# Performance work log

Hardware: AMD Instinct MI355X
Metric: run time of the kernel (lower is better)

Reference implementation:

```python
import jax, jax.numpy as jnp
from jax import lax
import numpy as np

# --- config (torchvision Mask R-CNN RPN / RoIAlign defaults) ---
IMG = 800.0        # image size (square)
STRIDE = 4.0       # FPN level stride -> feature 200x200
K_PRE = 2000       # pre-NMS top-k proposals
K_POST = 512       # post-NMS proposals kept
IOU_THR = 0.7      # RPN NMS IoU threshold
OUT = 7            # RoIAlign output size
SR = 2             # RoIAlign sampling ratio
SCALE = 1.0 / STRIDE
BBOX_XFORM_CLIP = 4.135166556742356  # log(1000/16)


def setup_inputs() -> dict:
    key = jax.random.key(0)
    k1, k2, k3 = jax.random.split(key, 3)
    C, H, W = 256, 200, 200
    feature = jax.random.normal(k1, (C, H, W), jnp.float32)
    # anchor grid: 3 sizes per location, stride 4 (proper geometric anchors)
    sizes = np.array([32.0, 64.0, 128.0], np.float32)
    ys, xs = np.meshgrid(np.arange(H, dtype=np.float32) * STRIDE,
                         np.arange(W, dtype=np.float32) * STRIDE, indexing='ij')
    ctr = np.stack([xs, ys], axis=-1).reshape(-1, 1, 2)            # [HW,1,2] (x,y)
    half = np.stack([sizes / 2, sizes / 2], axis=-1)[None]          # [1,3,2]
    anchors = np.concatenate([ctr - half + 0 * half, ctr + half], axis=-1)
    anchors = np.broadcast_to(np.concatenate([ctr - half, ctr + half], -1),
                              (H * W, 3, 4)).reshape(-1, 4).astype(np.float32)
    N = anchors.shape[0]  # 120000
    objectness = jax.random.normal(k2, (N,), jnp.float32)
    deltas = jax.random.normal(k3, (N, 4), jnp.float32) * 0.1
    return {"feature": feature, "objectness": objectness,
            "deltas": deltas, "anchors": jnp.asarray(anchors)}


def decode_boxes(deltas, anchors):
    w = anchors[:, 2] - anchors[:, 0]
    h = anchors[:, 3] - anchors[:, 1]
    cx = anchors[:, 0] + 0.5 * w
    cy = anchors[:, 1] + 0.5 * h
    dx, dy = deltas[:, 0], deltas[:, 1]
    dw = jnp.minimum(deltas[:, 2], BBOX_XFORM_CLIP)
    dh = jnp.minimum(deltas[:, 3], BBOX_XFORM_CLIP)
    pcx = dx * w + cx
    pcy = dy * h + cy
    pw = jnp.exp(dw) * w
    ph = jnp.exp(dh) * h
    boxes = jnp.stack([pcx - 0.5 * pw, pcy - 0.5 * ph,
                       pcx + 0.5 * pw, pcy + 0.5 * ph], axis=-1)
    return jnp.clip(boxes, 0.0, IMG)


def pairwise_iou(b):  # b: [K,4]
    area = (b[:, 2] - b[:, 0]) * (b[:, 3] - b[:, 1])
    lt = jnp.maximum(b[:, None, :2], b[None, :, :2])
    rb = jnp.minimum(b[:, None, 2:], b[None, :, 2:])
    wh = jnp.maximum(rb - lt, 0.0)
    inter = wh[..., 0] * wh[..., 1]
    return inter / (area[:, None] + area[None, :] - inter + 1e-6)


def nms_suppress(boxes_sorted, iou_thr):
    # boxes sorted by descending score; returns keep mask [K]
    K = boxes_sorted.shape[0]
    iou = pairwise_iou(boxes_sorted)
    js = jnp.arange(K)
    def body(i, supp):
        row = (iou[i] > iou_thr) & (js > i)
        return jnp.where(supp[i], supp, supp | row)
    supp = lax.fori_loop(0, K, body, jnp.zeros((K,), bool))
    return ~supp


def roi_align(feature, boxes):
    # feature: [C,H,W]; boxes: [M,4] in image coords; aligned=False variant
    C, H, W = feature.shape
    P = OUT * SR
    def one(box):
        x1, y1, x2, y2 = box[0] * SCALE, box[1] * SCALE, box[2] * SCALE, box[3] * SCALE
        rw = jnp.maximum(x2 - x1, 1.0)
        rh = jnp.maximum(y2 - y1, 1.0)
        idx = jnp.arange(P, dtype=feature.dtype) + 0.5
        ys = y1 + idx * (rh / P)   # [P]
        xs = x1 + idx * (rw / P)
        yy, xx = jnp.meshgrid(ys, xs, indexing='ij')     # [P,P]
        y = jnp.clip(yy, 0.0, H - 1.0)
        x = jnp.clip(xx, 0.0, W - 1.0)
        y0 = jnp.floor(y).astype(jnp.int32)
        x0 = jnp.floor(x).astype(jnp.int32)
        y1i = jnp.minimum(y0 + 1, H - 1)
        x1i = jnp.minimum(x0 + 1, W - 1)
        ly = y - y0.astype(feature.dtype)
        lx = x - x0.astype(feature.dtype)
        v00 = feature[:, y0, x0]    # [C,P,P]
        v01 = feature[:, y0, x1i]
        v10 = feature[:, y1i, x0]
        v11 = feature[:, y1i, x1i]
        val = (v00 * (1 - ly) * (1 - lx) + v01 * (1 - ly) * lx
               + v10 * ly * (1 - lx) + v11 * ly * lx)  # [C,P,P]
        return val.reshape(C, OUT, SR, OUT, SR).mean(axis=(2, 4))  # [C,7,7]
    return jax.vmap(one)(boxes)


def reference(feature, objectness, deltas, anchors):
    boxes = decode_boxes(deltas, anchors)                    # [N,4]
    scores, idx = lax.top_k(objectness, K_PRE)               # pre-NMS top-k
    cand = boxes[idx]                                        # [K_PRE,4] sorted
    keep = nms_suppress(cand, IOU_THR)                       # [K_PRE] bool
    masked = jnp.where(keep, scores, -jnp.inf)
    _, fidx = lax.top_k(masked, K_POST)                      # post-NMS top-k
    final_boxes = cand[fidx]                                 # [K_POST,4]
    valid = keep[fidx].astype(feature.dtype)                 # [K_POST]
    roi = roi_align(feature, final_boxes)                    # [K_POST,256,7,7]
    return roi * valid[:, None, None, None]
```

## Files before the change

### kernel.cpp

```cpp
#include <hip/hip_runtime.h>
#include <cstdint>
#include <cstddef>

#define N_ANCH   120000
#define K_PRE    2000
#define K_POST   512
#define CAP      4096
#define NWORD    32
#define HBINS    4096
#define IOU_THR  0.7f
#define IMGF     800.0f
#define CLIPV    4.135166556742356f
#define FH       200
#define FW       200
#define FC       256
#define SCALE    0.25f

#define TROWS    96
#define NTILE    21
#define CH       8

#define CG       16
#define TPE      4


typedef unsigned long long u64;
typedef float f2u __attribute__((ext_vector_type(2), aligned(4)));

struct Ws {
    uint32_t T;
    uint32_t cnt;
    int32_t  nk;
    uint32_t pad;
    u64      combo[CAP];
    float4   cand[K_PRE];
    int      rows[K_POST];
    u64      mask[(size_t)K_PRE * NWORD];
};

__device__ inline uint32_t fkey(float f) {
    uint32_t u = __float_as_uint(f);
    return (u & 0x80000000u) ? ~u : (u | 0x80000000u);
}

__global__ __launch_bounds__(1024) void zero_k(Ws* __restrict__ ws) {
    uint32_t* h = (uint32_t*)ws->mask;
    for (int i = threadIdx.x; i < HBINS; i += 1024) h[i] = 0u;
    if (threadIdx.x == 0) { ws->cnt = 0u; ws->nk = 0; ws->T = 0u; }
}

__global__ __launch_bounds__(256) void th_k(const float* __restrict__ feat,
                                            const float* __restrict__ obj,
                                            float* __restrict__ featT,
                                            uint32_t* __restrict__ hist) {
    __shared__ float tile[32][257];
    __shared__ uint32_t h[HBINS];
    const int tid = threadIdx.x, bid = blockIdx.x;

    if (bid < 118) {
        for (int i = tid; i < HBINS; i += 256) h[i] = 0u;
        __syncthreads();
        const int i = bid * 256 + tid;
        if (i < N_ANCH / 4) {
            float4 v = ((const float4*)obj)[i];
            atomicAdd(&h[fkey(v.x) >> 20], 1u);
            atomicAdd(&h[fkey(v.y) >> 20], 1u);
            atomicAdd(&h[fkey(v.z) >> 20], 1u);
            atomicAdd(&h[fkey(v.w) >> 20], 1u);
        }
        __syncthreads();
        for (int i2 = tid; i2 < HBINS; i2 += 256)
            if (h[i2]) atomicAdd(&hist[i2], h[i2]);
    }

    const int P0 = bid * 32;
    const int pl = tid & 31, c0 = tid >> 5;
#pragma unroll
    for (int k = 0; k < 32; ++k)
        tile[pl][k * 8 + c0] = feat[(size_t)(k * 8 + c0) * (FH * FW) + P0 + pl];
    __syncthreads();
#pragma unroll
    for (int m = 0; m < 32; ++m)
        featT[(size_t)(P0 + m) * FC + tid] = tile[m][tid];
}

__global__ __launch_bounds__(256) void hist_k(const float* __restrict__ obj,
                                              uint32_t* __restrict__ hist) {
    __shared__ uint32_t h[HBINS];
    for (int i = threadIdx.x; i < HBINS; i += 256) h[i] = 0u;
    __syncthreads();
    const float4* o4 = (const float4*)obj;
    for (int i = blockIdx.x * 256 + threadIdx.x; i < N_ANCH / 4; i += gridDim.x * 256) {
        float4 v = o4[i];
        atomicAdd(&h[fkey(v.x) >> 20], 1u);
        atomicAdd(&h[fkey(v.y) >> 20], 1u);
        atomicAdd(&h[fkey(v.z) >> 20], 1u);
        atomicAdd(&h[fkey(v.w) >> 20], 1u);
    }
    __syncthreads();
    for (int i = threadIdx.x; i < HBINS; i += 256)
        if (h[i]) atomicAdd(&hist[i], h[i]);
}

__global__ __launch_bounds__(256) void gather_k(const float* __restrict__ obj,
                                                const uint32_t* __restrict__ hist,
                                                Ws* __restrict__ ws) {
    __shared__ uint32_t wsum[4];
    __shared__ uint32_t sT;
    const int tid = threadIdx.x;
    const int lane = tid & 63, wave = tid >> 6;
    uint32_t c[16]; uint32_t s = 0;
#pragma unroll
    for (int k = 0; k < 16; ++k) { c[k] = hist[HBINS - 1 - (16 * tid + k)]; s += c[k]; }
    uint32_t incl = s;
    for (int off = 1; off < 64; off <<= 1) {
        uint32_t t = __shfl_up(incl, off);
        if (lane >= off) incl += t;
    }
    if (lane == 63) wsum[wave] = incl;
    __syncthreads();
    uint32_t wpre = 0;
    for (int w2 = 0; w2 < wave; ++w2) wpre += wsum[w2];
    uint32_t before = wpre + incl - s;
#pragma unroll
    for (int k = 0; k < 16; ++k) {
        uint32_t after = before + c[k];
        if (before < K_PRE && after >= K_PRE)
            sT = (uint32_t)(HBINS - 1 - (16 * tid + k)) << 20;
        before = after;
    }
    __syncthreads();
    const uint32_t T = sT;
    int i = blockIdx.x * 256 + tid;
    if (i >= N_ANCH / 4) return;
    float4 v = ((const float4*)obj)[i];
    float vals[4] = {v.x, v.y, v.z, v.w};
#pragma unroll
    for (int k = 0; k < 4; ++k) {
        uint32_t u = fkey(vals[k]);
        if (u >= T) {
            uint32_t pos = atomicAdd(&ws->cnt, 1u);
            if (pos < CAP)
                ws->combo[pos] = ((u64)(~u) << 32) | (uint32_t)(4 * i + k);
        }
    }
}

__global__ __launch_bounds__(256) void rank_decode_k(const float* __restrict__ deltas,
                                                     const float* __restrict__ anchors,
                                                     Ws* __restrict__ ws) {
    __shared__ u64 sc[CAP];
    const int tid = threadIdx.x;
    int M = (int)ws->cnt;
    if (M > CAP) M = CAP;
    const int ebase = blockIdx.x * (256 / TPE);
    if (ebase >= M) return;
    for (int e = tid; e < M; e += 256) sc[e] = ws->combo[e];
    __syncthreads();
    const int gid = ebase + tid / TPE;
    const int sub = tid & (TPE - 1);
    if (gid >= M) return;
    const u64 mine = sc[gid];
    int cnt = 0;
    int j = sub;
    for (; j + 3 * TPE < M; j += 4 * TPE) {
        u64 a = sc[j], b = sc[j + TPE], c = sc[j + 2 * TPE], d = sc[j + 3 * TPE];
        cnt += (int)(a < mine) + (int)(b < mine) + (int)(c < mine) + (int)(d < mine);
    }
    for (; j < M; j += TPE) cnt += (int)(sc[j] < mine);
    cnt += __shfl_xor(cnt, 1);
    cnt += __shfl_xor(cnt, 2);
    if (sub == 0 && cnt < K_PRE) {
        const uint32_t idx = (uint32_t)(mine & 0xFFFFFFFFull);
        float a0 = anchors[idx * 4 + 0], a1 = anchors[idx * 4 + 1];
        float a2 = anchors[idx * 4 + 2], a3 = anchors[idx * 4 + 3];
        float d0 = deltas[idx * 4 + 0],  d1 = deltas[idx * 4 + 1];
        float d2 = fminf(deltas[idx * 4 + 2], CLIPV);
        float d3 = fminf(deltas[idx * 4 + 3], CLIPV);
        float w = a2 - a0, h = a3 - a1;
        float cx = a0 + 0.5f * w, cy = a1 + 0.5f * h;
        float pcx = d0 * w + cx, pcy = d1 * h + cy;
        float pw = expf(d2) * w, ph = expf(d3) * h;
        float x1 = fminf(fmaxf(pcx - 0.5f * pw, 0.0f), IMGF);
        float y1 = fminf(fmaxf(pcy - 0.5f * ph, 0.0f), IMGF);
        float x2 = fminf(fmaxf(pcx + 0.5f * pw, 0.0f), IMGF);
        float y2 = fminf(fmaxf(pcy + 0.5f * ph, 0.0f), IMGF);
        ws->cand[cnt] = make_float4(x1, y1, x2, y2);
    }
}

__global__ __launch_bounds__(256) void nms_mask_k(Ws* __restrict__ ws) {
    const int i = blockIdx.x;
    const int lane = threadIdx.x & 63;
    const int wave = threadIdx.x >> 6;
    const float4 bi = ws->cand[i];
    const float ai = (bi.z - bi.x) * (bi.w - bi.y);
    for (int wd = wave; wd < NWORD; wd += 4) {
        int j = wd * 64 + lane;
        bool bit = false;
        if (j < K_PRE && j > i) {
            float4 bj = ws->cand[j];
            float aj = (bj.z - bj.x) * (bj.w - bj.y);
            float xx1 = fmaxf(bi.x, bj.x);
            float yy1 = fmaxf(bi.y, bj.y);
            float xx2 = fminf(bi.z, bj.z);
            float yy2 = fminf(bi.w, bj.w);
            float ww = fmaxf(xx2 - xx1, 0.0f);
            float hh = fmaxf(yy2 - yy1, 0.0f);
            float inter = ww * hh;
            float iou = inter / (ai + aj - inter + 1e-6f);
            bit = iou > IOU_THR;
        }
        u64 bal = __ballot(bit);
        if (lane == 0) ws->mask[(size_t)i * NWORD + wd] = bal;
    }
}

__global__ __launch_bounds__(512) void nms_scan_k(Ws* __restrict__ ws) {
    __shared__ __align__(16) u64 sbuf[2][TROWS * NWORD];
    __shared__ int s_stop;
    const int tid = threadIdx.x;
    const int lane = tid & 63;
    const int wave = tid >> 6;
    const int lmod = lane & 31;
    const u64* __restrict__ mask = ws->mask;

    {
        const ulonglong2* src = (const ulonglong2*)mask;
        ulonglong2* dst = (ulonglong2*)sbuf[0];
        for (int e = tid; e < TROWS * NWORD / 2; e += 512) dst[e] = src[e];
    }
    if (tid == 0) s_stop = 0;
    __syncthreads();

    u64 supp = 0ull;
    int kcnt = 0;
    int decided = 0;
    for (int t = 0; t < NTILE; ++t) {
        const int base = t * TROWS;
        const int nb = min(TROWS, K_PRE - base);
        if (wave == 0) {
            const u64* sm = sbuf[t & 1];
            u64 A[CH], B[CH];
#pragma unroll
            for (int b = 0; b < CH; ++b) A[b] = sm[b * NWORD + lmod];
            for (int s = 0; s < nb; s += 2 * CH) {
                const bool hasB = (s + CH) < nb;
                if (hasB) {
#pragma unroll
                    for (int b = 0; b < CH; ++b) B[b] = sm[(s + CH + b) * NWORD + lmod];
                }
                {
                    const int w = (base + s) >> 6;
                    const int bofs = (base + s) & 63;
                    u64 keptw = 0ull;
                    if (lane == w) {
                        u64 cur = supp;
#pragma unroll
                        for (int b = 0; b < CH; ++b) {
                            u64 bit = (cur >> (bofs + b)) & 1ull;
                            u64 sel = bit - 1ull;
                            cur |= A[b] & sel;
                            keptw |= sel & (1ull << b);
                        }
                        supp = cur;
                    }
                    u64 kb = __shfl(keptw, w);
                    kcnt += __popcll(kb);
#pragma unroll
                    for (int b = 0; b < CH; ++b) {
                        u64 sel = 0ull - ((kb >> b) & 1ull);
                        supp |= A[b] & sel;
                    }
                }
                if (hasB) {
                    if (s + 2 * CH < nb) {
#pragma unroll
                        for (int b = 0; b < CH; ++b)
                            A[b] = sm[(s + 2 * CH + b) * NWORD + lmod];
                    }
                    const int w = (base + s + CH) >> 6;
                    const int bofs = (base + s + CH) & 63;
                    u64 keptw = 0ull;
                    if (lane == w) {
                        u64 cur = supp;
#pragma unroll
                        for (int b = 0; b < CH; ++b) {
                            u64 bit = (cur >> (bofs + b)) & 1ull;
                            u64 sel = bit - 1ull;
                            cur |= B[b] & sel;
                            keptw |= sel & (1ull << b);
                        }
                        supp = cur;
                    }
                    u64 kb = __shfl(keptw, w);
                    kcnt += __popcll(kb);
#pragma unroll
                    for (int b = 0; b < CH; ++b) {
                        u64 sel = 0ull - ((kb >> b) & 1ull);
                        supp |= B[b] & sel;
                    }
                }
            }
            decided = base + nb;
            if (lane == 0 && kcnt >= K_POST) s_stop = 1;
        } else if (t + 1 < NTILE) {
            const int nbase = (t + 1) * TROWS;
            const int npairs = (min(TROWS, K_PRE - nbase) * NWORD) / 2;
            const ulonglong2* src = (const ulonglong2*)(mask + (size_t)nbase * NWORD);
            ulonglong2* dst = (ulonglong2*)sbuf[(t + 1) & 1];
            for (int e = tid - 64; e < npairs; e += 448) dst[e] = src[e];
        }
        __syncthreads();
        if (s_stop) break;
    }

    if (wave == 0) {
        u64 valid;
        if (lane < NWORD - 1)       valid = ~0ull;
        else if (lane == NWORD - 1) valid = (1ull << (K_PRE - (NWORD - 1) * 64)) - 1ull;
        else                        valid = 0ull;
        const int dw = decided - lane * 64;
        const u64 dmask = (dw <= 0) ? 0ull : ((dw >= 64) ? ~0ull : ((1ull << dw) - 1ull));
        u64 keepw = (~supp) & valid & dmask;
        int cnt = __popcll(keepw);
        int incl = cnt;
        for (int off = 1; off < 64; off <<= 1) {
            int t = __shfl_up(incl, off);
            if (lane >= off) incl += t;
        }
        int pos = incl - cnt;
        u64 kw = keepw;
        while (kw) {
            int b = __ffsll((unsigned long long)kw) - 1;
            kw &= kw - 1ull;
            if (pos < K_POST) ws->rows[pos] = lane * 64 + b;
            ++pos;
        }
        int total = __shfl(incl, 63);
        if (lane == 0) ws->nk = total;
        int start = total < K_POST ? total : K_POST;
        for (int r = start + lane; r < K_POST; r += 64) ws->rows[r] = -1;
    }
}

__global__ __launch_bounds__(256) void roi2_k(const float* __restrict__ featT,
                                              const Ws* __restrict__ ws,
                                              float* __restrict__ out) {
    __shared__ float sout[CG * 49];
    const int b = blockIdx.x;
    const int xcd = b & 7;
    const int s = b >> 3;
    const int r = s & (K_POST - 1);
    const int cg = xcd + 8 * (s >> 9);
    const int cbase = cg * CG;
    float* oblk = out + (size_t)r * (FC * 49) + (size_t)cbase * 49;
    const int row = ws->rows[r];
    const int tid = threadIdx.x;

    if (row < 0) {
        for (int e = tid; e < CG * 49; e += 256) oblk[e] = 0.0f;
        return;
    }

    if (tid < 196) {
        const int p = tid >> 2;
        const int cq = tid & 3;
        const int oy = p / 7, ox = p % 7;

        const float4 bx = ws->cand[row];
        const float x1 = bx.x * SCALE, y1 = bx.y * SCALE;
        const float x2 = bx.z * SCALE, y2 = bx.w * SCALE;
        const float rw = fmaxf(x2 - x1, 1.0f);
        const float rh = fmaxf(y2 - y1, 1.0f);
        const float stepx = rw / 14.0f;
        const float stepy = rh / 14.0f;

        int    o0[4], o1[4];
        float4 w4[4];
#pragma unroll
        for (int sub = 0; sub < 4; ++sub) {
            const int sy = sub >> 1, sx = sub & 1;
            float yy = y1 + ((float)(2 * oy + sy) + 0.5f) * stepy;
            float y = fminf(fmaxf(yy, 0.0f), (float)(FH - 1));
            float fy0 = floorf(y);
            int iy0 = (int)fy0;
            int iy1 = min(iy0 + 1, FH - 1);
            float ly = y - fy0;
            float xx = x1 + ((float)(2 * ox + sx) + 0.5f) * stepx;
            float x = fminf(fmaxf(xx, 0.0f), (float)(FW - 1));
            float fx0 = floorf(x);
            int ix0 = (int)fx0;
            float lx = x - fx0;
            float wxl, wxr; int basex;
            if (ix0 >= FW - 1) { basex = FW - 2; wxl = 0.0f; wxr = 1.0f; }
            else               { basex = ix0;    wxl = 1.0f - lx; wxr = lx; }
            float wy0 = 1.0f - ly, wy1 = ly;
            o0[sub] = (iy0 * FW + basex) * FC;
            o1[sub] = (iy1 * FW + basex) * FC;
            w4[sub] = make_float4(wy0 * wxl * 0.25f, wy0 * wxr * 0.25f,
                                  wy1 * wxl * 0.25f, wy1 * wxr * 0.25f);
        }

        const int cofs = cbase + cq * 4;
        float4 v[16];
#pragma unroll
        for (int sub = 0; sub < 4; ++sub) {
            v[4 * sub + 0] = *(const float4*)(featT + (size_t)o0[sub] + cofs);
            v[4 * sub + 1] = *(const float4*)(featT + (size_t)o0[sub] + FC + cofs);
            v[4 * sub + 2] = *(const float4*)(featT + (size_t)o1[sub] + cofs);
            v[4 * sub + 3] = *(const float4*)(featT + (size_t)o1[sub] + FC + cofs);
        }

        float ax = 0.0f, ay = 0.0f, az = 0.0f, aw = 0.0f;
#pragma unroll
        for (int sub = 0; sub < 4; ++sub) {
            const float4 w = w4[sub];
            ax += w.x * v[4*sub].x + w.y * v[4*sub+1].x + w.z * v[4*sub+2].x + w.w * v[4*sub+3].x;
            ay += w.x * v[4*sub].y + w.y * v[4*sub+1].y + w.z * v[4*sub+2].y + w.w * v[4*sub+3].y;
            az += w.x * v[4*sub].z + w.y * v[4*sub+1].z + w.z * v[4*sub+2].z + w.w * v[4*sub+3].z;
            aw += w.x * v[4*sub].w + w.y * v[4*sub+1].w + w.z * v[4*sub+2].w + w.w * v[4*sub+3].w;
        }
        sout[(cq * 4 + 0) * 49 + p] = ax;
        sout[(cq * 4 + 1) * 49 + p] = ay;
        sout[(cq * 4 + 2) * 49 + p] = az;
        sout[(cq * 4 + 3) * 49 + p] = aw;
    }
    __syncthreads();
    for (int e = tid; e < CG * 49; e += 256) oblk[e] = sout[e];
}

__global__ __launch_bounds__(256) void roi_k(const float* __restrict__ feat,
                                             const Ws* __restrict__ ws,
                                             float* __restrict__ out) {
    const int b = blockIdx.x;
    const int xcd = b & 7;
    const int s = b >> 3;
    const int r = s & (K_POST - 1);
    const int cg = xcd + 8 * (s >> 9);
    const int cbase = cg * CG;
    float* oblk = out + (size_t)r * (FC * 49) + (size_t)cbase * 49;
    const int row = ws->rows[r];
    const int tid = threadIdx.x;

    if (row < 0) {
        for (int e = tid; e < CG * 49; e += 256) oblk[e] = 0.0f;
        return;
    }
    if (tid >= 245) return;

    const int p = tid % 49;
    const int cslot = tid / 49;
    const int oy = p / 7, ox = p % 7;

    const float4 bx = ws->cand[row];
    const float x1 = bx.x * SCALE, y1 = bx.y * SCALE;
    const float x2 = bx.z * SCALE, y2 = bx.w * SCALE;
    const float rw = fmaxf(x2 - x1, 1.0f);
    const float rh = fmaxf(y2 - y1, 1.0f);
    const float stepx = rw / 14.0f;
    const float stepy = rh / 14.0f;

    int    off0[4], off1[4];
    float4 w4[4];
#pragma unroll
    for (int sub = 0; sub < 4; ++sub) {
        const int sy = sub >> 1, sx = sub & 1;
        float yy = y1 + ((float)(2 * oy + sy) + 0.5f) * stepy;
        float y = fminf(fmaxf(yy, 0.0f), (float)(FH - 1));
        float fy0 = floorf(y);
        int iy0 = (int)fy0;
        int iy1 = min(iy0 + 1, FH - 1);
        float ly = y - fy0;
        float xx = x1 + ((float)(2 * ox + sx) + 0.5f) * stepx;
        float x = fminf(fmaxf(xx, 0.0f), (float)(FW - 1));
        float fx0 = floorf(x);
        int ix0 = (int)fx0;
        float lx = x - fx0;
        float wxl, wxr; int base;
        if (ix0 >= FW - 1) { base = FW - 2; wxl = 0.0f; wxr = 1.0f; }
        else               { base = ix0;    wxl = 1.0f - lx; wxr = lx; }
        float wy0 = 1.0f - ly, wy1 = ly;
        off0[sub] = iy0 * FW + base;
        off1[sub] = iy1 * FW + base;
        w4[sub] = make_float4(wy0 * wxl * 0.25f, wy0 * wxr * 0.25f,
                              wy1 * wxl * 0.25f, wy1 * wxr * 0.25f);
    }

    const float* fb = feat + (size_t)cbase * (FH * FW);
    const float* f0 = fb + (size_t)cslot * (FH * FW);
    const float* f1 = fb + (size_t)(cslot + 5) * (FH * FW);
    const float* f2 = fb + (size_t)(cslot + 10) * (FH * FW);
    f2u r0[8], r1[8], r2[8], r3[8];
#pragma unroll
    for (int sub = 0; sub < 4; ++sub) {
        r0[2 * sub]     = *(const f2u*)(f0 + off0[sub]);
        r0[2 * sub + 1] = *(const f2u*)(f0 + off1[sub]);
    }
#pragma unroll
    for (int sub = 0; sub < 4; ++sub) {
        r1[2 * sub]     = *(const f2u*)(f1 + off0[sub]);
        r1[2 * sub + 1] = *(const f2u*)(f1 + off1[sub]);
    }
#pragma unroll
    for (int sub = 0; sub < 4; ++sub) {
        r2[2 * sub]     = *(const f2u*)(f2 + off0[sub]);
        r2[2 * sub + 1] = *(const f2u*)(f2 + off1[sub]);
    }
    const bool has4 = (cslot == 0);
    if (has4) {
        const float* f3 = fb + (size_t)15 * (FH * FW);
#pragma unroll
        for (int sub = 0; sub < 4; ++sub) {
            r3[2 * sub]     = *(const f2u*)(f3 + off0[sub]);
            r3[2 * sub + 1] = *(const f2u*)(f3 + off1[sub]);
        }
    }

    float a0 = 0.0f, a1 = 0.0f, a2 = 0.0f;
#pragma unroll
    for (int sub = 0; sub < 4; ++sub) {
        a0 += w4[sub].x * r0[2 * sub].x + w4[sub].y * r0[2 * sub].y
            + w4[sub].z * r0[2 * sub + 1].x + w4[sub].w * r0[2 * sub + 1].y;
    }
#pragma unroll
    for (int sub = 0; sub < 4; ++sub) {
        a1 += w4[sub].x * r1[2 * sub].x + w4[sub].y * r1[2 * sub].y
            + w4[sub].z * r1[2 * sub + 1].x + w4[sub].w * r1[2 * sub + 1].y;
    }
#pragma unroll
    for (int sub = 0; sub < 4; ++sub) {
        a2 += w4[sub].x * r2[2 * sub].x + w4[sub].y * r2[2 * sub].y
            + w4[sub].z * r2[2 * sub + 1].x + w4[sub].w * r2[2 * sub + 1].y;
    }
    oblk[cslot * 49 + p] = a0;
    oblk[(cslot + 5) * 49 + p] = a1;
    oblk[(cslot + 10) * 49 + p] = a2;

    if (has4) {
        float a3 = 0.0f;
#pragma unroll
        for (int sub = 0; sub < 4; ++sub) {
            a3 += w4[sub].x * r3[2 * sub].x + w4[sub].y * r3[2 * sub].y
                + w4[sub].z * r3[2 * sub + 1].x + w4[sub].w * r3[2 * sub + 1].y;
        }
        oblk[15 * 49 + p] = a3;
    }
}

extern "C" void kernel_launch(void* const* d_in, const int* in_sizes, int n_in,
                              void* d_out, int out_size, void* d_ws, size_t ws_size,
                              hipStream_t stream) {
    const float* feature    = (const float*)d_in[0];
    const float* objectness = (const float*)d_in[1];
    const float* deltas     = (const float*)d_in[2];
    const float* anchors    = (const float*)d_in[3];
    Ws* ws = (Ws*)d_ws;
    uint32_t* hist = (uint32_t*)ws->mask;
    float* out = (float*)d_out;

    const size_t ftOff = (sizeof(Ws) + 255) & ~(size_t)255;
    const size_t need  = ftOff + (size_t)(FH * FW) * FC * sizeof(float);
    const bool hwc = (ws_size >= need);
    float* featT = (float*)((char*)d_ws + ftOff);

    hipLaunchKernelGGL(zero_k, dim3(1), dim3(1024), 0, stream, ws);
    if (hwc) {
        hipLaunchKernelGGL(th_k, dim3(FH * FW / 32), dim3(256), 0, stream,
                           feature, objectness, featT, hist);
    } else {
        hipLaunchKernelGGL(hist_k, dim3(256), dim3(256), 0, stream, objectness, hist);
    }
    hipLaunchKernelGGL(gather_k, dim3((N_ANCH / 4 + 255) / 256), dim3(256), 0, stream,
                       objectness, hist, ws);
    hipLaunchKernelGGL(rank_decode_k, dim3(CAP / (256 / TPE)), dim3(256), 0, stream,
                       deltas, anchors, ws);
    hipLaunchKernelGGL(nms_mask_k, dim3(K_PRE), dim3(256), 0, stream, ws);
    hipLaunchKernelGGL(nms_scan_k, dim3(1), dim3(512), 0, stream, ws);
    if (hwc) {
        hipLaunchKernelGGL(roi2_k, dim3(16 * K_POST), dim3(256), 0, stream,
                           featT, ws, out);
    } else {
        hipLaunchKernelGGL(roi_k, dim3(16 * K_POST), dim3(256), 0, stream,
                           feature, ws, out);
    }
}
```

Measured before the change: 208.0 us.

## Overlap feature transpose with serial NMS scan in one fused launch

Moves the CHW-to-HWC feature transpose out of the early histogram kernel and into a new combined kernel. In that kernel, block 0 runs the single-block serial NMS scan at raised priority while the remaining blocks do the transpose. The goal is to hide the mostly idle single-block scan behind bandwidth-bound transpose work and to take the transpose off the front of the pipeline. The cost is that the transpose blocks compete with the latency-critical scan block for memory bandwidth and CU time, and the histogram now uses the separate hist_k launch.

```diff
diff --git a/kernel.cpp b/kernel.cpp
--- a/kernel.cpp
+++ b/kernel.cpp
@@ -47,41 +47,6 @@
     uint32_t* h = (uint32_t*)ws->mask;
     for (int i = threadIdx.x; i < HBINS; i += 1024) h[i] = 0u;
     if (threadIdx.x == 0) { ws->cnt = 0u; ws->nk = 0; ws->T = 0u; }
-}
-
-__global__ __launch_bounds__(256) void th_k(const float* __restrict__ feat,
-                                            const float* __restrict__ obj,
-                                            float* __restrict__ featT,
-                                            uint32_t* __restrict__ hist) {
-    __shared__ float tile[32][257];
-    __shared__ uint32_t h[HBINS];
-    const int tid = threadIdx.x, bid = blockIdx.x;
-
-    if (bid < 118) {
-        for (int i = tid; i < HBINS; i += 256) h[i] = 0u;
-        __syncthreads();
-        const int i = bid * 256 + tid;
-        if (i < N_ANCH / 4) {
-            float4 v = ((const float4*)obj)[i];
-            atomicAdd(&h[fkey(v.x) >> 20], 1u);
-            atomicAdd(&h[fkey(v.y) >> 20], 1u);
-            atomicAdd(&h[fkey(v.z) >> 20], 1u);
-            atomicAdd(&h[fkey(v.w) >> 20], 1u);
-        }
-        __syncthreads();
-        for (int i2 = tid; i2 < HBINS; i2 += 256)
-            if (h[i2]) atomicAdd(&hist[i2], h[i2]);
-    }
-
-    const int P0 = bid * 32;
-    const int pl = tid & 31, c0 = tid >> 5;
-#pragma unroll
-    for (int k = 0; k < 32; ++k)
-        tile[pl][k * 8 + c0] = feat[(size_t)(k * 8 + c0) * (FH * FW) + P0 + pl];
-    __syncthreads();
-#pragma unroll
-    for (int m = 0; m < 32; ++m)
-        featT[(size_t)(P0 + m) * FC + tid] = tile[m][tid];
 }
 
 __global__ __launch_bounds__(256) void hist_k(const float* __restrict__ obj,
@@ -216,6 +181,160 @@
     }
 }
 
+__global__ __launch_bounds__(512) void scan_t_k(const float* __restrict__ feat,
+                                                float* __restrict__ featT,
+                                                Ws* __restrict__ ws) {
+    __shared__ union __align__(16) {
+        u64   sbuf[2][TROWS * NWORD];
+        float tile[32][257];
+    } sm;
+    __shared__ int s_stop;
+    const int tid = threadIdx.x;
+    const int lane = tid & 63;
+    const int wave = tid >> 6;
+
+    if (blockIdx.x != 0) {
+        const int P0 = ((int)blockIdx.x - 1) * 32;
+        const int pl = tid & 31;
+        const int c0 = tid >> 5;
+#pragma unroll
+        for (int k = 0; k < 16; ++k) {
+            const int ch = k * 16 + c0;
+            sm.tile[pl][ch] = feat[(size_t)ch * (FH * FW) + P0 + pl];
+        }
+        __syncthreads();
+        const int half = tid >> 8;
+        const int col = tid & 255;
+#pragma unroll
+        for (int mm = 0; mm < 16; ++mm) {
+            const int row = 2 * mm + half;
+            featT[(size_t)(P0 + row) * FC + col] = sm.tile[row][col];
+        }
+        return;
+    }
+
+    __builtin_amdgcn_s_setprio(2);
+    const int lmod = lane & 31;
+    const u64* __restrict__ mask = ws->mask;
+    {
+        const ulonglong2* src = (const ulonglong2*)mask;
+        ulonglong2* dst = (ulonglong2*)sm.sbuf[0];
+        for (int e = tid; e < TROWS * NWORD / 2; e += 512) dst[e] = src[e];
+    }
+    if (tid == 0) s_stop = 0;
+    __syncthreads();
+
+    u64 supp = 0ull;
+    int kcnt = 0;
+    int decided = 0;
+    for (int t = 0; t < NTILE; ++t) {
+        const int base = t * TROWS;
+        const int nb = min(TROWS, K_PRE - base);
+        if (wave == 0) {
+            const u64* smb = sm.sbuf[t & 1];
+            u64 A[CH], B[CH];
+#pragma unroll
+            for (int b = 0; b < CH; ++b) A[b] = smb[b * NWORD + lmod];
+            for (int s = 0; s < nb; s += 2 * CH) {
+                const bool hasB = (s + CH) < nb;
+                if (hasB) {
+#pragma unroll
+                    for (int b = 0; b < CH; ++b) B[b] = smb[(s + CH + b) * NWORD + lmod];
+                }
+                {
+                    const int w = (base + s) >> 6;
+                    const int bofs = (base + s) & 63;
+                    u64 keptw = 0ull;
+                    if (lane == w) {
+                        u64 cur = supp;
+#pragma unroll
+                        for (int b = 0; b < CH; ++b) {
+                            u64 bit = (cur >> (bofs + b)) & 1ull;
+                            u64 sel = bit - 1ull;
+                            cur |= A[b] & sel;
+                            keptw |= sel & (1ull << b);
+                        }
+                        supp = cur;
+                    }
+                    u64 kb = __shfl(keptw, w);
+                    kcnt += __popcll(kb);
+#pragma unroll
+                    for (int b = 0; b < CH; ++b) {
+                        u64 sel = 0ull - ((kb >> b) & 1ull);
+                        supp |= A[b] & sel;
+                    }
+                }
+                if (hasB) {
+                    if (s + 2 * CH < nb) {
+#pragma unroll
+                        for (int b = 0; b < CH; ++b)
+                            A[b] = smb[(s + 2 * CH + b) * NWORD + lmod];
+                    }
+                    const int w = (base + s + CH) >> 6;
+                    const int bofs = (base + s + CH) & 63;
+                    u64 keptw = 0ull;
+                    if (lane == w) {
+                        u64 cur = supp;
+#pragma unroll
+                        for (int b = 0; b < CH; ++b) {
+                            u64 bit = (cur >> (bofs + b)) & 1ull;
+                            u64 sel = bit - 1ull;
+                            cur |= B[b] & sel;
+                            keptw |= sel & (1ull << b);
+                        }
+                        supp = cur;
+                    }
+                    u64 kb = __shfl(keptw, w);
+                    kcnt += __popcll(kb);
+#pragma unroll
+                    for (int b = 0; b < CH; ++b) {
+                        u64 sel = 0ull - ((kb >> b) & 1ull);
+                        supp |= B[b] & sel;
+                    }
+                }
+            }
+            decided = base + nb;
+            if (lane == 0 && kcnt >= K_POST) s_stop = 1;
+        } else if (t + 1 < NTILE) {
+            const int nbase = (t + 1) * TROWS;
+            const int npairs = (min(TROWS, K_PRE - nbase) * NWORD) / 2;
+            const ulonglong2* src = (const ulonglong2*)(mask + (size_t)nbase * NWORD);
+            ulonglong2* dst = (ulonglong2*)sm.sbuf[(t + 1) & 1];
+            for (int e = tid - 64; e < npairs; e += 448) dst[e] = src[e];
+        }
+        __syncthreads();
+        if (s_stop) break;
+    }
+
+    if (wave == 0) {
+        u64 valid;
+        if (lane < NWORD - 1)       valid = ~0ull;
+        else if (lane == NWORD - 1) valid = (1ull << (K_PRE - (NWORD - 1) * 64)) - 1ull;
+        else                        valid = 0ull;
+        const int dw = decided - lane * 64;
+        const u64 dmask = (dw <= 0) ? 0ull : ((dw >= 64) ? ~0ull : ((1ull << dw) - 1ull));
+        u64 keepw = (~supp) & valid & dmask;
+        int cnt = __popcll(keepw);
+        int incl = cnt;
+        for (int off = 1; off < 64; off <<= 1) {
+            int t = __shfl_up(incl, off);
+            if (lane >= off) incl += t;
+        }
+        int pos = incl - cnt;
+        u64 kw = keepw;
+        while (kw) {
+            int b = __ffsll((unsigned long long)kw) - 1;
+            kw &= kw - 1ull;
+            if (pos < K_POST) ws->rows[pos] = lane * 64 + b;
+            ++pos;
+        }
+        int total = __shfl(incl, 63);
+        if (lane == 0) ws->nk = total;
+        int start = total < K_POST ? total : K_POST;
+        for (int r = start + lane; r < K_POST; r += 64) ws->rows[r] = -1;
+    }
+}
+
 __global__ __launch_bounds__(512) void nms_scan_k(Ws* __restrict__ ws) {
     __shared__ __align__(16) u64 sbuf[2][TROWS * NWORD];
     __shared__ int s_stop;
@@ -565,22 +684,19 @@
     float* featT = (float*)((char*)d_ws + ftOff);
 
     hipLaunchKernelGGL(zero_k, dim3(1), dim3(1024), 0, stream, ws);
-    if (hwc) {
-        hipLaunchKernelGGL(th_k, dim3(FH * FW / 32), dim3(256), 0, stream,
-                           feature, objectness, featT, hist);
-    } else {
-        hipLaunchKernelGGL(hist_k, dim3(256), dim3(256), 0, stream, objectness, hist);
-    }
+    hipLaunchKernelGGL(hist_k, dim3(256), dim3(256), 0, stream, objectness, hist);
     hipLaunchKernelGGL(gather_k, dim3((N_ANCH / 4 + 255) / 256), dim3(256), 0, stream,
                        objectness, hist, ws);
     hipLaunchKernelGGL(rank_decode_k, dim3(CAP / (256 / TPE)), dim3(256), 0, stream,
                        deltas, anchors, ws);
     hipLaunchKernelGGL(nms_mask_k, dim3(K_PRE), dim3(256), 0, stream, ws);
-    hipLaunchKernelGGL(nms_scan_k, dim3(1), dim3(512), 0, stream, ws);
     if (hwc) {
+        hipLaunchKernelGGL(scan_t_k, dim3(1 + FH * FW / 32), dim3(512), 0, stream,
+                           feature, featT, ws);
         hipLaunchKernelGGL(roi2_k, dim3(16 * K_POST), dim3(256), 0, stream,
                            featT, ws, out);
     } else {
+        hipLaunchKernelGGL(nms_scan_k, dim3(1), dim3(512), 0, stream, ws);
         hipLaunchKernelGGL(roi_k, dim3(16 * K_POST), dim3(256), 0, stream,
                            feature, ws, out);
     }
```

Result: faster. 199.3 us (-4.2%).

## Drop zero kernel via bin-partitioned histogram; fuse feature transpose into NMS mask kernel

Applied to the files above, without the earlier changes.

The histogram kernel now gives each of 32 blocks ownership of 128 bins. Each block scans all objectness values and writes its bins directly, which removes the global zeroing kernel and the global atomics. The HWC feature transpose moves out of the histogram kernel and into the NMS mask kernel as extra blocks, so the transpose overlaps with the IoU mask work and one launch is saved. The cost is that every histogram block re-reads the whole objectness array, and ws->T is no longer reset.

```diff
diff --git a/kernel.cpp b/kernel.cpp
--- a/kernel.cpp
+++ b/kernel.cpp
@@ -43,63 +43,29 @@
     return (u & 0x80000000u) ? ~u : (u | 0x80000000u);
 }
 
-__global__ __launch_bounds__(1024) void zero_k(Ws* __restrict__ ws) {
-    uint32_t* h = (uint32_t*)ws->mask;
-    for (int i = threadIdx.x; i < HBINS; i += 1024) h[i] = 0u;
-    if (threadIdx.x == 0) { ws->cnt = 0u; ws->nk = 0; ws->T = 0u; }
-}
-
-__global__ __launch_bounds__(256) void th_k(const float* __restrict__ feat,
-                                            const float* __restrict__ obj,
-                                            float* __restrict__ featT,
-                                            uint32_t* __restrict__ hist) {
-    __shared__ float tile[32][257];
-    __shared__ uint32_t h[HBINS];
+__global__ __launch_bounds__(256) void hist_k(const float* __restrict__ obj,
+                                              uint32_t* __restrict__ hist,
+                                              Ws* __restrict__ ws) {
+    __shared__ uint32_t h[128];
     const int tid = threadIdx.x, bid = blockIdx.x;
-
-    if (bid < 118) {
-        for (int i = tid; i < HBINS; i += 256) h[i] = 0u;
-        __syncthreads();
-        const int i = bid * 256 + tid;
-        if (i < N_ANCH / 4) {
-            float4 v = ((const float4*)obj)[i];
-            atomicAdd(&h[fkey(v.x) >> 20], 1u);
-            atomicAdd(&h[fkey(v.y) >> 20], 1u);
-            atomicAdd(&h[fkey(v.z) >> 20], 1u);
-            atomicAdd(&h[fkey(v.w) >> 20], 1u);
-        }
-        __syncthreads();
-        for (int i2 = tid; i2 < HBINS; i2 += 256)
-            if (h[i2]) atomicAdd(&hist[i2], h[i2]);
-    }
-
-    const int P0 = bid * 32;
-    const int pl = tid & 31, c0 = tid >> 5;
-#pragma unroll
-    for (int k = 0; k < 32; ++k)
-        tile[pl][k * 8 + c0] = feat[(size_t)(k * 8 + c0) * (FH * FW) + P0 + pl];
-    __syncthreads();
-#pragma unroll
-    for (int m = 0; m < 32; ++m)
-        featT[(size_t)(P0 + m) * FC + tid] = tile[m][tid];
-}
-
-__global__ __launch_bounds__(256) void hist_k(const float* __restrict__ obj,
-                                              uint32_t* __restrict__ hist) {
-    __shared__ uint32_t h[HBINS];
-    for (int i = threadIdx.x; i < HBINS; i += 256) h[i] = 0u;
-    __syncthreads();
+    if (tid < 128) h[tid] = 0u;
+    if (bid == 0 && tid == 0) { ws->cnt = 0u; ws->nk = 0; }
+    __syncthreads();
+    const uint32_t lo = (uint32_t)bid << 7;
     const float4* o4 = (const float4*)obj;
-    for (int i = blockIdx.x * 256 + threadIdx.x; i < N_ANCH / 4; i += gridDim.x * 256) {
+    for (int i = tid; i < N_ANCH / 4; i += 256) {
         float4 v = o4[i];
-        atomicAdd(&h[fkey(v.x) >> 20], 1u);
-        atomicAdd(&h[fkey(v.y) >> 20], 1u);
-        atomicAdd(&h[fkey(v.z) >> 20], 1u);
-        atomicAdd(&h[fkey(v.w) >> 20], 1u);
-    }
-    __syncthreads();
-    for (int i = threadIdx.x; i < HBINS; i += 256)
-        if (h[i]) atomicAdd(&hist[i], h[i]);
+        uint32_t b0 = fkey(v.x) >> 20;
+        uint32_t b1 = fkey(v.y) >> 20;
+        uint32_t b2 = fkey(v.z) >> 20;
+        uint32_t b3 = fkey(v.w) >> 20;
+        if ((b0 & ~127u) == lo) atomicAdd(&h[b0 & 127u], 1u);
+        if ((b1 & ~127u) == lo) atomicAdd(&h[b1 & 127u], 1u);
+        if ((b2 & ~127u) == lo) atomicAdd(&h[b2 & 127u], 1u);
+        if ((b3 & ~127u) == lo) atomicAdd(&h[b3 & 127u], 1u);
+    }
+    __syncthreads();
+    if (tid < 128) hist[lo + tid] = h[tid];
 }
 
 __global__ __launch_bounds__(256) void gather_k(const float* __restrict__ obj,
@@ -187,6 +153,51 @@
         float y2 = fminf(fmaxf(pcy + 0.5f * ph, 0.0f), IMGF);
         ws->cand[cnt] = make_float4(x1, y1, x2, y2);
     }
+}
+
+__global__ __launch_bounds__(256) void mask_t_k(const float* __restrict__ feat,
+                                                float* __restrict__ featT,
+                                                Ws* __restrict__ ws) {
+    __shared__ float tile[32][257];
+    const int tid = threadIdx.x;
+
+    if (blockIdx.x < K_PRE) {
+        const int i = blockIdx.x;
+        const int lane = tid & 63;
+        const int wave = tid >> 6;
+        const float4 bi = ws->cand[i];
+        const float ai = (bi.z - bi.x) * (bi.w - bi.y);
+        for (int wd = wave; wd < NWORD; wd += 4) {
+            int j = wd * 64 + lane;
+            bool bit = false;
+            if (j < K_PRE && j > i) {
+                float4 bj = ws->cand[j];
+                float aj = (bj.z - bj.x) * (bj.w - bj.y);
+                float xx1 = fmaxf(bi.x, bj.x);
+                float yy1 = fmaxf(bi.y, bj.y);
+                float xx2 = fminf(bi.z, bj.z);
+                float yy2 = fminf(bi.w, bj.w);
+                float ww = fmaxf(xx2 - xx1, 0.0f);
+                float hh = fmaxf(yy2 - yy1, 0.0f);
+                float inter = ww * hh;
+                float iou = inter / (ai + aj - inter + 1e-6f);
+                bit = iou > IOU_THR;
+            }
+            u64 bal = __ballot(bit);
+            if (lane == 0) ws->mask[(size_t)i * NWORD + wd] = bal;
+        }
+        return;
+    }
+
+    const int P0 = ((int)blockIdx.x - K_PRE) * 32;
+    const int pl = tid & 31, c0 = tid >> 5;
+#pragma unroll
+    for (int k = 0; k < 32; ++k)
+        tile[pl][k * 8 + c0] = feat[(size_t)(k * 8 + c0) * (FH * FW) + P0 + pl];
+    __syncthreads();
+#pragma unroll
+    for (int m = 0; m < 32; ++m)
+        featT[(size_t)(P0 + m) * FC + tid] = tile[m][tid];
 }
 
 __global__ __launch_bounds__(256) void nms_mask_k(Ws* __restrict__ ws) {
@@ -564,23 +575,21 @@
     const bool hwc = (ws_size >= need);
     float* featT = (float*)((char*)d_ws + ftOff);
 
-    hipLaunchKernelGGL(zero_k, dim3(1), dim3(1024), 0, stream, ws);
-    if (hwc) {
-        hipLaunchKernelGGL(th_k, dim3(FH * FW / 32), dim3(256), 0, stream,
-                           feature, objectness, featT, hist);
-    } else {
-        hipLaunchKernelGGL(hist_k, dim3(256), dim3(256), 0, stream, objectness, hist);
-    }
+    hipLaunchKernelGGL(hist_k, dim3(HBINS / 128), dim3(256), 0, stream,
+                       objectness, hist, ws);
     hipLaunchKernelGGL(gather_k, dim3((N_ANCH / 4 + 255) / 256), dim3(256), 0, stream,
                        objectness, hist, ws);
     hipLaunchKernelGGL(rank_decode_k, dim3(CAP / (256 / TPE)), dim3(256), 0, stream,
                        deltas, anchors, ws);
-    hipLaunchKernelGGL(nms_mask_k, dim3(K_PRE), dim3(256), 0, stream, ws);
-    hipLaunchKernelGGL(nms_scan_k, dim3(1), dim3(512), 0, stream, ws);
     if (hwc) {
+        hipLaunchKernelGGL(mask_t_k, dim3(K_PRE + FH * FW / 32), dim3(256), 0, stream,
+                           feature, featT, ws);
+        hipLaunchKernelGGL(nms_scan_k, dim3(1), dim3(512), 0, stream, ws);
         hipLaunchKernelGGL(roi2_k, dim3(16 * K_POST), dim3(256), 0, stream,
                            featT, ws, out);
     } else {
+        hipLaunchKernelGGL(nms_mask_k, dim3(K_PRE), dim3(256), 0, stream, ws);
+        hipLaunchKernelGGL(nms_scan_k, dim3(1), dim3(512), 0, stream, ws);
         hipLaunchKernelGGL(roi_k, dim3(16 * K_POST), dim3(256), 0, stream,
                            feature, ws, out);
     }
```

After: 251.9 us. 1.21x slower.
